# Kernel tuning notes

Measured on AMD Instinct MI355X. Metric: run time of the kernel, lower is better.

## Reference

```python
import jax, jax.numpy as jnp
import numpy as np


def setup_inputs() -> dict:
    key = jax.random.key(0)
    k1, k2 = jax.random.split(key)
    B, D, N = 8, 3, 4096
    srcs = jax.random.normal(k1, (B, D, N), dtype=jnp.float32)
    tgts = jax.random.normal(k2, (B, D, N), dtype=jnp.float32)
    return {"srcs": srcs, "tgts": tgts}


def _chamfer(srcs, tgts):
    # srcs, tgts: [B, D, N] -> points [B, N, D]
    s = jnp.swapaxes(srcs, 1, 2)  # [B, Ns, D]
    t = jnp.swapaxes(tgts, 1, 2)  # [B, Nt, D]
    # squared norms (equals diag of self-distance bmm in original)
    rs = jnp.sum(s * s, axis=-1)  # [B, Ns]
    rt = jnp.sum(t * t, axis=-1)  # [B, Nt]
    st = jnp.einsum("bnd,bmd->bnm", s, t)  # [B, Ns, Nt]
    # P[b,i,j] = |s_i|^2 + |t_j|^2 - 2 s_i . t_j
    P = rs[:, :, None] + rt[:, None, :] - 2.0 * st
    # min over src dim (axis 1) mean + min over tgt dim (axis 2) mean
    return jnp.min(P, axis=1).mean() + jnp.min(P, axis=2).mean()


def reference(srcs, tgts):
    return _chamfer(srcs, tgts)
```

## Files before the change

### kernel.cpp

```cpp
#include <hip/hip_runtime.h>


#define CD_B 8
#define CD_N 4096
#define BLK 256
#define TCH 16
#define TPB (CD_N / TCH)
#define QQ 8
#define QPB (BLK * QQ)
#define QCH (CD_N / QPB)
#define NQ (2 * CD_B * CD_N)

__global__ __launch_bounds__(BLK) void cd_partial(
    const float* __restrict__ srcs, const float* __restrict__ tgts,
    float* __restrict__ ws, float* __restrict__ out) {
  const int bid = blockIdx.x;
  const int tc  = bid & (TCH - 1);
  const int qc  = (bid >> 4) & (QCH - 1);
  const int b   = (bid >> 5) & (CD_B - 1);
  const int dir = bid >> 8;

  const float* qb = (dir ? tgts : srcs) + b * 3 * CD_N;
  const float* tb = (dir ? srcs : tgts) + b * 3 * CD_N;

  __shared__ float4 T[TPB];
  const int tid = threadIdx.x;
  {
    int gj = tc * TPB + tid;
    float x = tb[gj], y = tb[CD_N + gj], z = tb[2 * CD_N + gj];
    T[tid] = make_float4(x, y, z, x * x + y * y + z * z);
  }
  if (bid == 0 && tid == 0) out[0] = 0.0f;
  __syncthreads();

  float sx[QQ], sy[QQ], sz[QQ];
  const int q0 = qc * QPB + tid;
#pragma unroll
  for (int qq = 0; qq < QQ; ++qq) {
    int q = q0 + qq * BLK;
    sx[qq] = qb[q];
    sy[qq] = qb[CD_N + q];
    sz[qq] = qb[2 * CD_N + q];
  }

  float mm[QQ];
#pragma unroll
  for (int qq = 0; qq < QQ; ++qq) mm[qq] = 3.4e38f;

  for (int j = 0; j < TPB; j += 2) {
#pragma unroll
    for (int u = 0; u < 2; ++u) {
      float4 p = T[j + u];
#pragma unroll
      for (int qq = 0; qq < QQ; ++qq) {
        float st = fmaf(sx[qq], p.x, fmaf(sy[qq], p.y, sz[qq] * p.z));
        mm[qq] = fminf(mm[qq], fmaf(-2.0f, st, p.w));
      }
    }
  }

  const int gqbase = (dir * CD_B + b) * CD_N + qc * QPB + tid;
  float* wrow = ws + (size_t)tc * NQ;
#pragma unroll
  for (int qq = 0; qq < QQ; ++qq) {
    float ssq = fmaf(sx[qq], sx[qq], fmaf(sy[qq], sy[qq], sz[qq] * sz[qq]));
    wrow[gqbase + qq * BLK] = mm[qq] + ssq;
  }
}

__global__ __launch_bounds__(BLK) void cd_reduce(
    const float* __restrict__ ws, float* __restrict__ out) {
  const int q = blockIdx.x * BLK + threadIdx.x;
  float m = ws[q];
#pragma unroll
  for (int tc = 1; tc < TCH; ++tc) m = fminf(m, ws[(size_t)tc * NQ + q]);

  for (int off = 32; off; off >>= 1) m += __shfl_down(m, off, 64);
  __shared__ float wsum[BLK / 64];
  if ((threadIdx.x & 63) == 0) wsum[threadIdx.x >> 6] = m;
  __syncthreads();
  if (threadIdx.x == 0) {
    float s = (wsum[0] + wsum[1]) + (wsum[2] + wsum[3]);
    atomicAdd(out, s * (1.0f / (float)(CD_B * CD_N)));
  }
}

extern "C" void kernel_launch(void* const* d_in, const int* in_sizes, int n_in,
                              void* d_out, int out_size, void* d_ws, size_t ws_size,
                              hipStream_t stream) {
  const float* srcs = (const float*)d_in[0];
  const float* tgts = (const float*)d_in[1];
  float* out = (float*)d_out;
  float* ws = (float*)d_ws;

  cd_partial<<<2 * CD_B * QCH * TCH, BLK, 0, stream>>>(srcs, tgts, ws, out);
  cd_reduce<<<NQ / BLK, BLK, 0, stream>>>(ws, out);
}
```

Baseline: 86.84 us.

## Compute each distance tile once and reduce row and column minima together

Replaces the two-direction pass, which computed every distance twice, with a single 128x128 tile pass per batch. Each thread holds an 8x8 register microtile and updates both row minima and column minima using v_min3, then reduces them across lanes with shuffles and through shared memory. This halves the pairwise arithmetic and drops the LDS broadcast of target points. The cost is a larger workspace (32 partials per query instead of 16) and a longer reduce kernel.

Measured after the change: 86.31 us. No clear change (-0.6%).

```diff
diff --git a/kernel.cpp b/kernel.cpp
--- a/kernel.cpp
+++ b/kernel.cpp
@@ -4,76 +4,128 @@
 #define CD_B 8
 #define CD_N 4096
 #define BLK 256
-#define TCH 16
-#define TPB (CD_N / TCH)
-#define QQ 8
-#define QPB (BLK * QQ)
-#define QCH (CD_N / QPB)
+#define TIL 128
+#define NT  (CD_N / TIL)
+#define QI 8
+#define QJ 8
 #define NQ (2 * CD_B * CD_N)
 
-__global__ __launch_bounds__(BLK) void cd_partial(
+__device__ __forceinline__ float min3f(float m, float a, float b) {
+  asm("v_min3_f32 %0, %1, %2, %0" : "+v"(m) : "v"(a), "v"(b));
+  return m;
+}
+
+__global__ __launch_bounds__(BLK) void cd_tile(
     const float* __restrict__ srcs, const float* __restrict__ tgts,
     float* __restrict__ ws, float* __restrict__ out) {
   const int bid = blockIdx.x;
-  const int tc  = bid & (TCH - 1);
-  const int qc  = (bid >> 4) & (QCH - 1);
-  const int b   = (bid >> 5) & (CD_B - 1);
-  const int dir = bid >> 8;
+  const int jt  = bid & (NT - 1);
+  const int it  = (bid >> 5) & (NT - 1);
+  const int b   = bid >> 10;
+  const int tid = threadIdx.x;
+  const int tx  = tid & 15;
+  const int ty  = tid >> 4;
 
-  const float* qb = (dir ? tgts : srcs) + b * 3 * CD_N;
-  const float* tb = (dir ? srcs : tgts) + b * 3 * CD_N;
+  if (bid == 0 && tid == 0) out[0] = 0.0f;
 
-  __shared__ float4 T[TPB];
-  const int tid = threadIdx.x;
-  {
-    int gj = tc * TPB + tid;
-    float x = tb[gj], y = tb[CD_N + gj], z = tb[2 * CD_N + gj];
-    T[tid] = make_float4(x, y, z, x * x + y * y + z * z);
-  }
-  if (bid == 0 && tid == 0) out[0] = 0.0f;
-  __syncthreads();
+  const float* sb = srcs + b * 3 * CD_N;
+  const float* tb = tgts + b * 3 * CD_N;
+  const int i0 = it * TIL + ty * QI;
+  const int j0 = jt * TIL + tx * QJ;
 
-  float sx[QQ], sy[QQ], sz[QQ];
-  const int q0 = qc * QPB + tid;
+  float sx[QI], sy[QI], sz[QI], sw[QI];
+  float ux[QJ], uy[QJ], uz[QJ], uw[QJ];
+  *(float4*)&sx[0] = *(const float4*)(sb + i0);
+  *(float4*)&sx[4] = *(const float4*)(sb + i0 + 4);
+  *(float4*)&sy[0] = *(const float4*)(sb + CD_N + i0);
+  *(float4*)&sy[4] = *(const float4*)(sb + CD_N + i0 + 4);
+  *(float4*)&sz[0] = *(const float4*)(sb + 2 * CD_N + i0);
+  *(float4*)&sz[4] = *(const float4*)(sb + 2 * CD_N + i0 + 4);
+  *(float4*)&ux[0] = *(const float4*)(tb + j0);
+  *(float4*)&ux[4] = *(const float4*)(tb + j0 + 4);
+  *(float4*)&uy[0] = *(const float4*)(tb + CD_N + j0);
+  *(float4*)&uy[4] = *(const float4*)(tb + CD_N + j0 + 4);
+  *(float4*)&uz[0] = *(const float4*)(tb + 2 * CD_N + j0);
+  *(float4*)&uz[4] = *(const float4*)(tb + 2 * CD_N + j0 + 4);
 #pragma unroll
-  for (int qq = 0; qq < QQ; ++qq) {
-    int q = q0 + qq * BLK;
-    sx[qq] = qb[q];
-    sy[qq] = qb[CD_N + q];
-    sz[qq] = qb[2 * CD_N + q];
+  for (int u = 0; u < QI; ++u)
+    sw[u] = fmaf(sx[u], sx[u], fmaf(sy[u], sy[u], sz[u] * sz[u]));
+#pragma unroll
+  for (int u = 0; u < QJ; ++u) {
+    uw[u] = fmaf(ux[u], ux[u], fmaf(uy[u], uy[u], uz[u] * uz[u]));
+    ux[u] *= -2.0f; uy[u] *= -2.0f; uz[u] *= -2.0f;
   }
 
-  float mm[QQ];
+  float rm[QI], cm[QJ];
 #pragma unroll
-  for (int qq = 0; qq < QQ; ++qq) mm[qq] = 3.4e38f;
+  for (int u = 0; u < QI; ++u) rm[u] = 3.4e38f;
+#pragma unroll
+  for (int u = 0; u < QJ; ++u) cm[u] = 3.4e38f;
 
-  for (int j = 0; j < TPB; j += 2) {
 #pragma unroll
-    for (int u = 0; u < 2; ++u) {
-      float4 p = T[j + u];
+  for (int i = 0; i < QI; i += 2) {
 #pragma unroll
-      for (int qq = 0; qq < QQ; ++qq) {
-        float st = fmaf(sx[qq], p.x, fmaf(sy[qq], p.y, sz[qq] * p.z));
-        mm[qq] = fminf(mm[qq], fmaf(-2.0f, st, p.w));
-      }
+    for (int j = 0; j < QJ; j += 2) {
+      float b00 = sw[i] + uw[j];
+      float b01 = sw[i] + uw[j + 1];
+      float b10 = sw[i + 1] + uw[j];
+      float b11 = sw[i + 1] + uw[j + 1];
+      float v00 = fmaf(sx[i], ux[j], fmaf(sy[i], uy[j], fmaf(sz[i], uz[j], b00)));
+      float v01 = fmaf(sx[i], ux[j+1], fmaf(sy[i], uy[j+1], fmaf(sz[i], uz[j+1], b01)));
+      float v10 = fmaf(sx[i+1], ux[j], fmaf(sy[i+1], uy[j], fmaf(sz[i+1], uz[j], b10)));
+      float v11 = fmaf(sx[i+1], ux[j+1], fmaf(sy[i+1], uy[j+1], fmaf(sz[i+1], uz[j+1], b11)));
+      rm[i]     = min3f(rm[i],     v00, v01);
+      rm[i + 1] = min3f(rm[i + 1], v10, v11);
+      cm[j]     = min3f(cm[j],     v00, v10);
+      cm[j + 1] = min3f(cm[j + 1], v01, v11);
     }
   }
 
-  const int gqbase = (dir * CD_B + b) * CD_N + qc * QPB + tid;
-  float* wrow = ws + (size_t)tc * NQ;
 #pragma unroll
-  for (int qq = 0; qq < QQ; ++qq) {
-    float ssq = fmaf(sx[qq], sx[qq], fmaf(sy[qq], sy[qq], sz[qq] * sz[qq]));
-    wrow[gqbase + qq * BLK] = mm[qq] + ssq;
+  for (int u = 0; u < QI; ++u) {
+    float r = rm[u];
+    r = fminf(r, __shfl_xor(r, 1, 64));
+    r = fminf(r, __shfl_xor(r, 2, 64));
+    r = fminf(r, __shfl_xor(r, 4, 64));
+    r = fminf(r, __shfl_xor(r, 8, 64));
+    rm[u] = r;
+  }
+  if (tx == 0) {
+    float* wrow = ws + (size_t)jt * NQ + b * CD_N + i0;
+    *(float4*)&wrow[0] = make_float4(rm[0], rm[1], rm[2], rm[3]);
+    *(float4*)&wrow[4] = make_float4(rm[4], rm[5], rm[6], rm[7]);
+  }
+
+#pragma unroll
+  for (int u = 0; u < QJ; ++u) {
+    float c = cm[u];
+    c = fminf(c, __shfl_xor(c, 16, 64));
+    c = fminf(c, __shfl_xor(c, 32, 64));
+    cm[u] = c;
+  }
+  __shared__ float C[4][TIL];
+  if ((ty & 3) == 0) {
+#pragma unroll
+    for (int u = 0; u < QJ; ++u) C[ty >> 2][tx * QJ + u] = cm[u];
+  }
+  __syncthreads();
+  if (tid < TIL) {
+    float c = fminf(fminf(C[0][tid], C[1][tid]), fminf(C[2][tid], C[3][tid]));
+    ws[(size_t)it * NQ + CD_B * CD_N + b * CD_N + jt * TIL + tid] = c;
   }
 }
 
 __global__ __launch_bounds__(BLK) void cd_reduce(
     const float* __restrict__ ws, float* __restrict__ out) {
   const int q = blockIdx.x * BLK + threadIdx.x;
-  float m = ws[q];
+  float m0 = ws[q];
+  float m1 = ws[(size_t)1 * NQ + q];
 #pragma unroll
-  for (int tc = 1; tc < TCH; ++tc) m = fminf(m, ws[(size_t)tc * NQ + q]);
+  for (int k = 2; k < NT; k += 2) {
+    m0 = fminf(m0, ws[(size_t)k * NQ + q]);
+    m1 = fminf(m1, ws[(size_t)(k + 1) * NQ + q]);
+  }
+  float m = fminf(m0, m1);
 
   for (int off = 32; off; off >>= 1) m += __shfl_down(m, off, 64);
   __shared__ float wsum[BLK / 64];
@@ -93,6 +145,6 @@
   float* out = (float*)d_out;
   float* ws = (float*)d_ws;
 
-  cd_partial<<<2 * CD_B * QCH * TCH, BLK, 0, stream>>>(srcs, tgts, ws, out);
+  cd_tile<<<CD_B * NT * NT, BLK, 0, stream>>>(srcs, tgts, ws, out);
   cd_reduce<<<NQ / BLK, BLK, 0, stream>>>(ws, out);
 }
```
